# Optimization experiments

Measured on AMD Instinct MI355X. Metric: run time of the kernel, lower is better.

## Reference

```python
import jax, jax.numpy as jnp
import numpy as np

N_NODES = 50000
N_EDGES = 400000
IN_FEATS = 16
HIDDEN = 32
EDGE_FEATS = 16
EDGE_MLP_HID = 8 * IN_FEATS  # 128
N_CLS_EDGES = 100000
OUT_FEATS = 2


def setup_inputs() -> dict:
    key = jax.random.key(0)
    ks = jax.random.split(key, 12)
    s = 0.05
    return {
        "node_feats": jax.random.normal(ks[0], (N_NODES, IN_FEATS), jnp.float32),
        "edge_feats": jax.random.normal(ks[1], (N_EDGES, EDGE_FEATS), jnp.float32),
        "src": jax.random.randint(ks[2], (N_EDGES,), 0, N_NODES),
        "dst": jax.random.randint(ks[3], (N_EDGES,), 0, N_NODES),
        "edge_indices": jax.random.randint(ks[4], (N_CLS_EDGES,), 0, N_EDGES),
        "en_w1": s * jax.random.normal(ks[5], (EDGE_FEATS, EDGE_MLP_HID), jnp.float32),
        "en_b1": jnp.zeros((EDGE_MLP_HID,), jnp.float32),
        "en_w2": s * jax.random.normal(ks[6], (EDGE_MLP_HID, HIDDEN * IN_FEATS), jnp.float32),
        "en_b2": jnp.zeros((HIDDEN * IN_FEATS,), jnp.float32),
        "conv_b": jnp.zeros((HIDDEN,), jnp.float32),
        "cls_w1": s * jax.random.normal(ks[7], (2 * HIDDEN + EDGE_FEATS, HIDDEN), jnp.float32),
        "cls_b1": jnp.zeros((HIDDEN,), jnp.float32),
        "cls_w2": s * jax.random.normal(ks[8], (HIDDEN, OUT_FEATS), jnp.float32),
        "cls_b2": jnp.zeros((OUT_FEATS,), jnp.float32),
    }


def reference(node_feats, edge_feats, src, dst, edge_indices,
              en_w1, en_b1, en_w2, en_b2, conv_b,
              cls_w1, cls_b1, cls_w2, cls_b2):
    # edge MLP -> per-edge weight matrices [E, in_feats, hidden]
    ew = jax.nn.relu(edge_feats @ en_w1 + en_b1) @ en_w2 + en_b2
    W = ew.reshape(-1, IN_FEATS, HIDDEN)
    # gather src features, per-edge matvec, mean-scatter to dst (DGL NNConv, aggregator='mean')
    msg = jnp.einsum('ei,eih->eh', node_feats[src], W)  # [E, hidden]
    agg = jax.ops.segment_sum(msg, dst, num_segments=N_NODES)
    deg = jax.ops.segment_sum(jnp.ones((N_EDGES,), msg.dtype), dst, num_segments=N_NODES)
    h = jax.nn.relu(agg / jnp.maximum(deg, 1.0)[:, None] + conv_b)  # dropout is identity at eval
    # edge classifier on selected edges
    s_idx = src[edge_indices]
    d_idx = dst[edge_indices]
    edge_input = jnp.concatenate([h[s_idx], h[d_idx], edge_feats[edge_indices]], axis=1)
    logits = jax.nn.relu(edge_input @ cls_w1 + cls_b1) @ cls_w2 + cls_b2
    return logits
```

## Files before the change

kernel.cpp:

```cpp
#include <hip/hip_runtime.h>
#include <stdint.h>

#define N_NODES   50000
#define N_EDGES   400000
#define IN_FEATS  16
#define HIDDEN    32
#define K1        128
#define NOUT      512
#define N_CLS     100000
#define CAP       40
#define TILE_E    128
#define FUSED_BLOCKS (N_EDGES / TILE_E)

typedef float  f32x4  __attribute__((ext_vector_type(4)));
typedef __bf16 bf16x8 __attribute__((ext_vector_type(8)));

__device__ __forceinline__ unsigned short f32_bf16(float f) {
    union { float f; uint32_t u; } c; c.f = f;
    uint32_t r = c.u + 0x7fffu + ((c.u >> 16) & 1u);
    return (unsigned short)(r >> 16);
}

__device__ __forceinline__ void gload_lds16(const unsigned short* g, unsigned short* l) {
    __builtin_amdgcn_global_load_lds(
        (const __attribute__((address_space(1))) unsigned int*)(g),
        (__attribute__((address_space(3))) unsigned int*)(l),
        16, 0, 0);
}

__global__ void prep_weights(const float* __restrict__ w2, const float* __restrict__ w1,
                             unsigned short* __restrict__ w2ts, unsigned short* __restrict__ w1t) {
    int tid = blockIdx.x * 256 + threadIdx.x;
    if (tid < NOUT * K1) {
        int n = tid >> 7, k = tid & 127;
        w2ts[n * 128 + (k ^ ((n & 7) << 3))] = f32_bf16(w2[k * 512 + n]);
    } else {
        int t = tid - NOUT * K1;
        int n = t >> 5, k = t & 31;
        w1t[n * 32 + k] = (k < 16) ? f32_bf16(w1[k * 128 + n]) : (unsigned short)0;
    }
}

__global__ void build_slots(const int* __restrict__ dst, int* __restrict__ cursor,
                            int* __restrict__ slots) {
    int e = blockIdx.x * 256 + threadIdx.x;
    if (e >= N_EDGES) return;
    int d = dst[e];
    int pos = atomicAdd(&cursor[d], 1);
    if (pos < CAP) slots[d * CAP + pos] = e;
}

__global__ __launch_bounds__(256, 4) void fused_msg(
    const float* __restrict__ nf, const float* __restrict__ ef,
    const int* __restrict__ src,
    const unsigned short* __restrict__ w1t, const float* __restrict__ b1,
    const unsigned short* __restrict__ w2ts, const float* __restrict__ b2,
    float* __restrict__ msg)
{
    __shared__ __align__(16) unsigned short sAmem[128 * 128];

    const int tid  = threadIdx.x;
    const int lane = tid & 63;
    const int w    = tid >> 6;
    const int l15  = lane & 15;
    const int lg   = lane >> 4;
    const int key  = (l15 & 7) << 3;
    const int e0   = blockIdx.x * TILE_E;

    unsigned short* buf0 = sAmem;
    unsigned short* buf1 = sAmem + 8192;

    auto stage = [&](int cc, unsigned short* buf) {
        #pragma unroll
        for (int i = 0; i < 4; ++i)
            gload_lds16(&w2ts[cc * 8192 + (w * 4 + i) * 512 + lane * 8],
                        &buf[(w * 4 + i) * 512]);
    };

    const int ea = e0 + w * 32 + l15;
    const int eb = ea + 16;
    const int sa0 = src[ea];
    const int sa1 = src[eb];

    {
        bf16x8 w1f0 = *reinterpret_cast<const bf16x8*>(&w1t[((2 * w) * 16 + l15) * 32 + lg * 8]);
        bf16x8 w1f1 = *reinterpret_cast<const bf16x8*>(&w1t[((2 * w + 1) * 16 + l15) * 32 + lg * 8]);
        float4 q0 = *reinterpret_cast<const float4*>(&b1[(2 * w) * 16 + lg * 4]);
        float4 q1 = *reinterpret_cast<const float4*>(&b1[(2 * w + 1) * 16 + lg * 4]);
        #pragma unroll
        for (int et = 0; et < 8; ++et) {
            int e = e0 + et * 16 + l15;
            bf16x8 aef;
            if (lg < 2) {
                float4 f0 = *reinterpret_cast<const float4*>(&ef[e * 16 + lg * 8]);
                float4 f1 = *reinterpret_cast<const float4*>(&ef[e * 16 + lg * 8 + 4]);
                unsigned short t8[8] = { f32_bf16(f0.x), f32_bf16(f0.y), f32_bf16(f0.z), f32_bf16(f0.w),
                                         f32_bf16(f1.x), f32_bf16(f1.y), f32_bf16(f1.z), f32_bf16(f1.w) };
                aef = *reinterpret_cast<const bf16x8*>(t8);
            } else {
                aef = bf16x8(0);
            }
            int le = et * 16 + l15;
            f32x4 c0 = { q0.x, q0.y, q0.z, q0.w };
            c0 = __builtin_amdgcn_mfma_f32_16x16x32_bf16(w1f0, aef, c0, 0, 0, 0);
            uint32_t u0 = (uint32_t)f32_bf16(fmaxf(c0[0], 0.f)) | ((uint32_t)f32_bf16(fmaxf(c0[1], 0.f)) << 16);
            uint32_t u1 = (uint32_t)f32_bf16(fmaxf(c0[2], 0.f)) | ((uint32_t)f32_bf16(fmaxf(c0[3], 0.f)) << 16);
            uint2 pk0 = { u0, u1 };
            *reinterpret_cast<uint2*>(&sAmem[le * 128 + (((2 * w) * 16 + lg * 4) ^ key)]) = pk0;

            f32x4 c1 = { q1.x, q1.y, q1.z, q1.w };
            c1 = __builtin_amdgcn_mfma_f32_16x16x32_bf16(w1f1, aef, c1, 0, 0, 0);
            uint32_t u2 = (uint32_t)f32_bf16(fmaxf(c1[0], 0.f)) | ((uint32_t)f32_bf16(fmaxf(c1[1], 0.f)) << 16);
            uint32_t u3 = (uint32_t)f32_bf16(fmaxf(c1[2], 0.f)) | ((uint32_t)f32_bf16(fmaxf(c1[3], 0.f)) << 16);
            uint2 pk1 = { u2, u3 };
            *reinterpret_cast<uint2*>(&sAmem[le * 128 + (((2 * w + 1) * 16 + lg * 4) ^ key)]) = pk1;
        }
    }
    __syncthreads();

    bf16x8 aF[2][4];
    #pragma unroll
    for (int et = 0; et < 2; ++et) {
        int le = w * 32 + et * 16 + l15;
        #pragma unroll
        for (int kb = 0; kb < 4; ++kb)
            aF[et][kb] = *reinterpret_cast<const bf16x8*>(
                &sAmem[le * 128 + ((kb * 32 + lg * 8) ^ key)]);
    }
    __syncthreads();

    stage(0, buf0);
    stage(1, buf1);
    __syncthreads();

    float msgv[2][8];
    #pragma unroll
    for (int et = 0; et < 2; ++et)
        #pragma unroll
        for (int q = 0; q < 8; ++q) msgv[et][q] = 0.f;

    #pragma unroll 1
    for (int c = 0; c < 8; ++c) {
        const unsigned short* sCur = (c & 1) ? buf1 : buf0;

        float2 xw0 = *reinterpret_cast<const float2*>(&nf[sa0 * 16 + c * 2]);
        float2 xw1 = *reinterpret_cast<const float2*>(&nf[sa1 * 16 + c * 2]);

        #pragma unroll
        for (int f = 0; f < 4; ++f) {
            int n = f * 16 + l15;
            bf16x8 bw[4];
            #pragma unroll
            for (int kb = 0; kb < 4; ++kb)
                bw[kb] = *reinterpret_cast<const bf16x8*>(
                    &sCur[n * 128 + ((kb * 32 + lg * 8) ^ key)]);
            float4 b2q = *reinterpret_cast<const float4*>(&b2[c * 64 + f * 16 + lg * 4]);
            f32x4 a0 = { b2q.x, b2q.y, b2q.z, b2q.w };
            f32x4 a1 = a0;
            #pragma unroll
            for (int kb = 0; kb < 4; ++kb) {
                a0 = __builtin_amdgcn_mfma_f32_16x16x32_bf16(bw[kb], aF[0][kb], a0, 0, 0, 0);
                a1 = __builtin_amdgcn_mfma_f32_16x16x32_bf16(bw[kb], aF[1][kb], a1, 0, 0, 0);
            }
            const float x0 = (f >> 1) ? xw0.y : xw0.x;
            const float x1 = (f >> 1) ? xw1.y : xw1.x;
            const int s = (f & 1) * 4;
            #pragma unroll
            for (int r = 0; r < 4; ++r) {
                msgv[0][s + r] += x0 * a0[r];
                msgv[1][s + r] += x1 * a1[r];
            }
        }

        if (c < 7) {
            __syncthreads();
            if (c + 2 < 8) stage(c + 2, (c & 1) ? buf1 : buf0);
        }
    }

    #pragma unroll
    for (int et = 0; et < 2; ++et) {
        int e = et ? eb : ea;
        #pragma unroll
        for (int half = 0; half < 2; ++half) {
            float4 o = { msgv[et][half * 4 + 0], msgv[et][half * 4 + 1],
                         msgv[et][half * 4 + 2], msgv[et][half * 4 + 3] };
            *reinterpret_cast<float4*>(&msg[e * 32 + half * 16 + lg * 4]) = o;
        }
    }
}

__global__ __launch_bounds__(256) void aggregate_h(
    const float* __restrict__ msg, const int* __restrict__ cursor,
    const int* __restrict__ slots, const float* __restrict__ conv_b,
    float* __restrict__ h)
{
    int t = blockIdx.x * 256 + threadIdx.x;
    int n = t >> 5;
    if (n >= N_NODES) return;
    int hh = t & 31;
    int d = cursor[n];
    int dm = d < CAP ? d : CAP;
    const int* row = &slots[n * CAP];
    float s = 0.f;
    int j = 0;
    for (; j + 4 <= dm; j += 4) {
        int ee0 = row[j], ee1 = row[j + 1], ee2 = row[j + 2], ee3 = row[j + 3];
        float v0 = msg[ee0 * 32 + hh], v1 = msg[ee1 * 32 + hh];
        float v2 = msg[ee2 * 32 + hh], v3 = msg[ee3 * 32 + hh];
        s += (v0 + v1) + (v2 + v3);
    }
    for (; j < dm; ++j) s += msg[row[j] * 32 + hh];
    h[n * 32 + hh] = fmaxf(s / fmaxf((float)d, 1.f) + conv_b[hh], 0.f);
}

__global__ __launch_bounds__(256) void classifier(
    const float* __restrict__ h, const float* __restrict__ ef,
    const int* __restrict__ src, const int* __restrict__ dst, const int* __restrict__ eidx,
    const float* __restrict__ w1, const float* __restrict__ b1,
    const float* __restrict__ w2, const float* __restrict__ b2, float* __restrict__ out)
{
    __shared__ float sIn[32][84];
    __shared__ float sW1[80 * 32];
    __shared__ float sHid[32][36];
    __shared__ int   sE[32 * 3];
    int tid = threadIdx.x;
    int eb  = blockIdx.x * 32;

    for (int i = tid; i < 640; i += 256)
        *reinterpret_cast<float4*>(&sW1[i * 4]) = *reinterpret_cast<const float4*>(&w1[i * 4]);
    if (tid < 32) {
        int ei = eidx[eb + tid];
        sE[tid * 3 + 0] = ei;
        sE[tid * 3 + 1] = src[ei];
        sE[tid * 3 + 2] = dst[ei];
    }
    __syncthreads();
    {
        int e = tid >> 3, l8 = tid & 7;
        int ei = sE[e * 3 + 0], sn = sE[e * 3 + 1], dn = sE[e * 3 + 2];
        #pragma unroll
        for (int j = 0; j < 10; ++j) {
            int c = l8 + j * 8;
            float v;
            if (c < 32)      v = h[sn * 32 + c];
            else if (c < 64) v = h[dn * 32 + (c - 32)];
            else             v = ef[ei * 16 + (c - 64)];
            sIn[e][c] = v;
        }
    }
    __syncthreads();
    {
        int e = tid >> 3, j0 = (tid & 7) * 4;
        float4 acc = *reinterpret_cast<const float4*>(&b1[j0]);
        #pragma unroll 8
        for (int k = 0; k < 80; ++k) {
            float x = sIn[e][k];
            float4 wv = *reinterpret_cast<const float4*>(&sW1[k * 32 + j0]);
            acc.x += x * wv.x; acc.y += x * wv.y; acc.z += x * wv.z; acc.w += x * wv.w;
        }
        sHid[e][j0 + 0] = fmaxf(acc.x, 0.f);
        sHid[e][j0 + 1] = fmaxf(acc.y, 0.f);
        sHid[e][j0 + 2] = fmaxf(acc.z, 0.f);
        sHid[e][j0 + 3] = fmaxf(acc.w, 0.f);
    }
    __syncthreads();
    if (tid < 64) {
        int e = tid >> 1, o = tid & 1;
        float acc = b2[o];
        #pragma unroll
        for (int j = 0; j < 32; ++j) acc += sHid[e][j] * w2[j * 2 + o];
        out[(eb + e) * 2 + o] = acc;
    }
}

extern "C" void kernel_launch(void* const* d_in, const int* in_sizes, int n_in,
                              void* d_out, int out_size, void* d_ws, size_t ws_size,
                              hipStream_t stream) {
    const float* nf     = (const float*)d_in[0];
    const float* ef     = (const float*)d_in[1];
    const int*   src    = (const int*)d_in[2];
    const int*   dst    = (const int*)d_in[3];
    const int*   eidx   = (const int*)d_in[4];
    const float* en_w1  = (const float*)d_in[5];
    const float* en_b1  = (const float*)d_in[6];
    const float* en_w2  = (const float*)d_in[7];
    const float* en_b2  = (const float*)d_in[8];
    const float* conv_b = (const float*)d_in[9];
    const float* cls_w1 = (const float*)d_in[10];
    const float* cls_b1 = (const float*)d_in[11];
    const float* cls_w2 = (const float*)d_in[12];
    const float* cls_b2 = (const float*)d_in[13];
    float* out = (float*)d_out;

    char* ws = (char*)d_ws;
    unsigned short* w2ts   = (unsigned short*)(ws);
    unsigned short* w1t    = (unsigned short*)(ws + 131072);
    int*            cursor = (int*)(ws + 139264);
    int*            slots  = (int*)(ws + 339264);
    float*          msgb   = (float*)(ws + 8339264);
    float*          h      = (float*)(ws + 59539264);

    hipMemsetAsync(cursor, 0, N_NODES * sizeof(int), stream);
    prep_weights<<<(NOUT * K1 + 4096) / 256, 256, 0, stream>>>(en_w2, en_w1, w2ts, w1t);
    build_slots<<<(N_EDGES + 255) / 256, 256, 0, stream>>>(dst, cursor, slots);
    fused_msg<<<FUSED_BLOCKS, 256, 0, stream>>>(nf, ef, src, w1t, en_b1, w2ts, en_b2, msgb);
    aggregate_h<<<(N_NODES * HIDDEN + 255) / 256, 256, 0, stream>>>(msgb, cursor, slots, conv_b, h);
    classifier<<<N_CLS / 32, 256, 0, stream>>>(h, ef, src, dst, eidx, cls_w1, cls_b1, cls_w2, cls_b2, out);
}
```

Baseline: 144.4 us.

## Split fused_msg work across input-feature halves and merge prep with slot building

Waves in fused_msg now each cover 64 edges and one half of the 16 input features, rather than 32 edges across all features. Each staged W2 fragment is therefore reused across four edge tiles, and the two partial messages are summed through LDS before a coalesced store. The weight swizzle key is widened to 16 rows to match the new access pattern. The weight preprocessing and slot-building kernels are merged into one launch. The price is more registers per thread (occupancy hint lowered from 4 to 3) and an extra LDS reduction pass with barriers.

```diff
diff --git a/kernel.cpp b/kernel.cpp
--- a/kernel.cpp
+++ b/kernel.cpp
@@ -28,29 +28,27 @@
         16, 0, 0);
 }
 
-__global__ void prep_weights(const float* __restrict__ w2, const float* __restrict__ w1,
-                             unsigned short* __restrict__ w2ts, unsigned short* __restrict__ w1t) {
-    int tid = blockIdx.x * 256 + threadIdx.x;
-    if (tid < NOUT * K1) {
-        int n = tid >> 7, k = tid & 127;
-        w2ts[n * 128 + (k ^ ((n & 7) << 3))] = f32_bf16(w2[k * 512 + n]);
-    } else {
-        int t = tid - NOUT * K1;
+__global__ void prep_and_slots(const float* __restrict__ w2, const float* __restrict__ w1,
+                               const int* __restrict__ dst,
+                               unsigned short* __restrict__ w2ts, unsigned short* __restrict__ w1t,
+                               int* __restrict__ cursor, int* __restrict__ slots) {
+    int gid = blockIdx.x * 256 + threadIdx.x;
+    if (gid < NOUT * K1) {
+        int n = gid >> 7, k = gid & 127;
+        w2ts[n * 128 + (k ^ ((n & 15) << 3))] = f32_bf16(w2[k * 512 + n]);
+    } else if (gid < NOUT * K1 + 4096) {
+        int t = gid - NOUT * K1;
         int n = t >> 5, k = t & 31;
         w1t[n * 32 + k] = (k < 16) ? f32_bf16(w1[k * 128 + n]) : (unsigned short)0;
     }
-}
-
-__global__ void build_slots(const int* __restrict__ dst, int* __restrict__ cursor,
-                            int* __restrict__ slots) {
-    int e = blockIdx.x * 256 + threadIdx.x;
-    if (e >= N_EDGES) return;
-    int d = dst[e];
-    int pos = atomicAdd(&cursor[d], 1);
-    if (pos < CAP) slots[d * CAP + pos] = e;
-}
-
-__global__ __launch_bounds__(256, 4) void fused_msg(
+    if (gid < N_EDGES) {
+        int d = dst[gid];
+        int pos = atomicAdd(&cursor[d], 1);
+        if (pos < CAP) slots[d * CAP + pos] = gid;
+    }
+}
+
+__global__ __launch_bounds__(256, 3) void fused_msg(
     const float* __restrict__ nf, const float* __restrict__ ef,
     const int* __restrict__ src,
     const unsigned short* __restrict__ w1t, const float* __restrict__ b1,
@@ -61,32 +59,37 @@
 
     const int tid  = threadIdx.x;
     const int lane = tid & 63;
-    const int w    = tid >> 6;
+    const int wid  = tid >> 6;
+    const int eh   = wid >> 1;
+    const int nh   = wid & 1;
     const int l15  = lane & 15;
     const int lg   = lane >> 4;
     const int key  = (l15 & 7) << 3;
+    const int key2 = l15 << 3;
     const int e0   = blockIdx.x * TILE_E;
 
-    unsigned short* buf0 = sAmem;
-    unsigned short* buf1 = sAmem + 8192;
-
-    auto stage = [&](int cc, unsigned short* buf) {
-        #pragma unroll
-        for (int i = 0; i < 4; ++i)
-            gload_lds16(&w2ts[cc * 8192 + (w * 4 + i) * 512 + lane * 8],
-                        &buf[(w * 4 + i) * 512]);
+    unsigned short* bufA = sAmem;
+    unsigned short* bufB = sAmem + 8192;
+
+    auto stage = [&](int s, unsigned short* buf) {
+        #pragma unroll
+        for (int i = 0; i < 4; ++i) {
+            int seg = wid * 4 + i;
+            int srcOff = (seg < 8) ? ((s * 32) * 128 + seg * 512)
+                                   : ((256 + s * 32) * 128 + (seg - 8) * 512);
+            gload_lds16(&w2ts[srcOff + lane * 8], &buf[seg * 512]);
+        }
     };
 
-    const int ea = e0 + w * 32 + l15;
-    const int eb = ea + 16;
-    const int sa0 = src[ea];
-    const int sa1 = src[eb];
+    int sa[4];
+    #pragma unroll
+    for (int et = 0; et < 4; ++et) sa[et] = src[e0 + eh * 64 + et * 16 + l15];
 
     {
-        bf16x8 w1f0 = *reinterpret_cast<const bf16x8*>(&w1t[((2 * w) * 16 + l15) * 32 + lg * 8]);
-        bf16x8 w1f1 = *reinterpret_cast<const bf16x8*>(&w1t[((2 * w + 1) * 16 + l15) * 32 + lg * 8]);
-        float4 q0 = *reinterpret_cast<const float4*>(&b1[(2 * w) * 16 + lg * 4]);
-        float4 q1 = *reinterpret_cast<const float4*>(&b1[(2 * w + 1) * 16 + lg * 4]);
+        bf16x8 w1f0 = *reinterpret_cast<const bf16x8*>(&w1t[((2 * wid) * 16 + l15) * 32 + lg * 8]);
+        bf16x8 w1f1 = *reinterpret_cast<const bf16x8*>(&w1t[((2 * wid + 1) * 16 + l15) * 32 + lg * 8]);
+        float4 q0 = *reinterpret_cast<const float4*>(&b1[(2 * wid) * 16 + lg * 4]);
+        float4 q1 = *reinterpret_cast<const float4*>(&b1[(2 * wid + 1) * 16 + lg * 4]);
         #pragma unroll
         for (int et = 0; et < 8; ++et) {
             int e = e0 + et * 16 + l15;
@@ -106,22 +109,22 @@
             uint32_t u0 = (uint32_t)f32_bf16(fmaxf(c0[0], 0.f)) | ((uint32_t)f32_bf16(fmaxf(c0[1], 0.f)) << 16);
             uint32_t u1 = (uint32_t)f32_bf16(fmaxf(c0[2], 0.f)) | ((uint32_t)f32_bf16(fmaxf(c0[3], 0.f)) << 16);
             uint2 pk0 = { u0, u1 };
-            *reinterpret_cast<uint2*>(&sAmem[le * 128 + (((2 * w) * 16 + lg * 4) ^ key)]) = pk0;
+            *reinterpret_cast<uint2*>(&sAmem[le * 128 + (((2 * wid) * 16 + lg * 4) ^ key)]) = pk0;
 
             f32x4 c1 = { q1.x, q1.y, q1.z, q1.w };
             c1 = __builtin_amdgcn_mfma_f32_16x16x32_bf16(w1f1, aef, c1, 0, 0, 0);
             uint32_t u2 = (uint32_t)f32_bf16(fmaxf(c1[0], 0.f)) | ((uint32_t)f32_bf16(fmaxf(c1[1], 0.f)) << 16);
             uint32_t u3 = (uint32_t)f32_bf16(fmaxf(c1[2], 0.f)) | ((uint32_t)f32_bf16(fmaxf(c1[3], 0.f)) << 16);
             uint2 pk1 = { u2, u3 };
-            *reinterpret_cast<uint2*>(&sAmem[le * 128 + (((2 * w + 1) * 16 + lg * 4) ^ key)]) = pk1;
-        }
-    }
-    __syncthreads();
-
-    bf16x8 aF[2][4];
-    #pragma unroll
-    for (int et = 0; et < 2; ++et) {
-        int le = w * 32 + et * 16 + l15;
+            *reinterpret_cast<uint2*>(&sAmem[le * 128 + (((2 * wid + 1) * 16 + lg * 4) ^ key)]) = pk1;
+        }
+    }
+    __syncthreads();
+
+    bf16x8 aF[4][4];
+    #pragma unroll
+    for (int et = 0; et < 4; ++et) {
+        int le = eh * 64 + et * 16 + l15;
         #pragma unroll
         for (int kb = 0; kb < 4; ++kb)
             aF[et][kb] = *reinterpret_cast<const bf16x8*>(
@@ -129,64 +132,82 @@
     }
     __syncthreads();
 
-    stage(0, buf0);
-    stage(1, buf1);
-    __syncthreads();
-
-    float msgv[2][8];
-    #pragma unroll
-    for (int et = 0; et < 2; ++et)
+    stage(0, bufA);
+    stage(1, bufB);
+    __syncthreads();
+
+    float msgv[4][8];
+    #pragma unroll
+    for (int et = 0; et < 4; ++et)
         #pragma unroll
         for (int q = 0; q < 8; ++q) msgv[et][q] = 0.f;
 
     #pragma unroll 1
-    for (int c = 0; c < 8; ++c) {
-        const unsigned short* sCur = (c & 1) ? buf1 : buf0;
-
-        float2 xw0 = *reinterpret_cast<const float2*>(&nf[sa0 * 16 + c * 2]);
-        float2 xw1 = *reinterpret_cast<const float2*>(&nf[sa1 * 16 + c * 2]);
-
-        #pragma unroll
-        for (int f = 0; f < 4; ++f) {
-            int n = f * 16 + l15;
+    for (int s = 0; s < 8; ++s) {
+        const unsigned short* sCur = (s & 1) ? bufB : bufA;
+        const int ib = nh * 8 + s;
+        float xv[4];
+        #pragma unroll
+        for (int et = 0; et < 4; ++et) xv[et] = nf[sa[et] * 16 + ib];
+
+        #pragma unroll
+        for (int f = 0; f < 2; ++f) {
+            int r = f * 16 + l15;
             bf16x8 bw[4];
             #pragma unroll
             for (int kb = 0; kb < 4; ++kb)
                 bw[kb] = *reinterpret_cast<const bf16x8*>(
-                    &sCur[n * 128 + ((kb * 32 + lg * 8) ^ key)]);
-            float4 b2q = *reinterpret_cast<const float4*>(&b2[c * 64 + f * 16 + lg * 4]);
+                    &sCur[nh * 4096 + r * 128 + ((kb * 32 + lg * 8) ^ key2)]);
+            float4 b2q = *reinterpret_cast<const float4*>(&b2[nh * 256 + s * 32 + f * 16 + lg * 4]);
             f32x4 a0 = { b2q.x, b2q.y, b2q.z, b2q.w };
-            f32x4 a1 = a0;
+            f32x4 a1 = a0, a2 = a0, a3 = a0;
             #pragma unroll
             for (int kb = 0; kb < 4; ++kb) {
                 a0 = __builtin_amdgcn_mfma_f32_16x16x32_bf16(bw[kb], aF[0][kb], a0, 0, 0, 0);
                 a1 = __builtin_amdgcn_mfma_f32_16x16x32_bf16(bw[kb], aF[1][kb], a1, 0, 0, 0);
+                a2 = __builtin_amdgcn_mfma_f32_16x16x32_bf16(bw[kb], aF[2][kb], a2, 0, 0, 0);
+                a3 = __builtin_amdgcn_mfma_f32_16x16x32_bf16(bw[kb], aF[3][kb], a3, 0, 0, 0);
             }
-            const float x0 = (f >> 1) ? xw0.y : xw0.x;
-            const float x1 = (f >> 1) ? xw1.y : xw1.x;
-            const int s = (f & 1) * 4;
+            const int sb = f * 4;
             #pragma unroll
-            for (int r = 0; r < 4; ++r) {
-                msgv[0][s + r] += x0 * a0[r];
-                msgv[1][s + r] += x1 * a1[r];
+            for (int rr = 0; rr < 4; ++rr) {
+                msgv[0][sb + rr] += xv[0] * a0[rr];
+                msgv[1][sb + rr] += xv[1] * a1[rr];
+                msgv[2][sb + rr] += xv[2] * a2[rr];
+                msgv[3][sb + rr] += xv[3] * a3[rr];
             }
         }
 
-        if (c < 7) {
+        if (s < 7) {
             __syncthreads();
-            if (c + 2 < 8) stage(c + 2, (c & 1) ? buf1 : buf0);
-        }
-    }
-
-    #pragma unroll
-    for (int et = 0; et < 2; ++et) {
-        int e = et ? eb : ea;
-        #pragma unroll
-        for (int half = 0; half < 2; ++half) {
-            float4 o = { msgv[et][half * 4 + 0], msgv[et][half * 4 + 1],
-                         msgv[et][half * 4 + 2], msgv[et][half * 4 + 3] };
-            *reinterpret_cast<float4*>(&msg[e * 32 + half * 16 + lg * 4]) = o;
-        }
+            if (s + 2 < 8) stage(s + 2, (s & 1) ? bufB : bufA);
+        }
+    }
+    __syncthreads();
+
+    float4* sPf4 = (float4*)sAmem;
+    #pragma unroll
+    for (int et = 0; et < 4; ++et) {
+        int el = eh * 64 + et * 16 + l15;
+        #pragma unroll
+        for (int f = 0; f < 2; ++f) {
+            int sl = (f * 4 + lg) ^ (el & 7);
+            float4 v = { msgv[et][f * 4 + 0], msgv[et][f * 4 + 1],
+                         msgv[et][f * 4 + 2], msgv[et][f * 4 + 3] };
+            sPf4[nh * 1024 + el * 8 + sl] = v;
+        }
+    }
+    __syncthreads();
+
+    #pragma unroll
+    for (int j = 0; j < 4; ++j) {
+        int idx = j * 256 + tid;
+        int e = idx >> 3, slot = idx & 7;
+        int sl = slot ^ (e & 7);
+        float4 v0 = sPf4[e * 8 + sl];
+        float4 v1 = sPf4[1024 + e * 8 + sl];
+        float4 o = { v0.x + v1.x, v0.y + v1.y, v0.z + v1.z, v0.w + v1.w };
+        *reinterpret_cast<float4*>(&msg[(e0 + e) * 32 + slot * 4]) = o;
     }
 }
 
@@ -302,8 +323,7 @@
     float*          h      = (float*)(ws + 59539264);
 
     hipMemsetAsync(cursor, 0, N_NODES * sizeof(int), stream);
-    prep_weights<<<(NOUT * K1 + 4096) / 256, 256, 0, stream>>>(en_w2, en_w1, w2ts, w1t);
-    build_slots<<<(N_EDGES + 255) / 256, 256, 0, stream>>>(dst, cursor, slots);
+    prep_and_slots<<<(N_EDGES + 255) / 256, 256, 0, stream>>>(en_w2, en_w1, dst, w2ts, w1t, cursor, slots);
     fused_msg<<<FUSED_BLOCKS, 256, 0, stream>>>(nf, ef, src, w1t, en_b1, w2ts, en_b2, msgb);
     aggregate_h<<<(N_NODES * HIDDEN + 255) / 256, 256, 0, stream>>>(msgb, cursor, slots, conv_b, h);
     classifier<<<N_CLS / 32, 256, 0, stream>>>(h, ef, src, dst, eidx, cls_w1, cls_b1, cls_w2, cls_b2, out);
```

Result: slower. 158.5 us (+9.7%).
